# Optimization experiments

Hardware: AMD Instinct MI355X
Metric: run time of the kernel (lower is better)

## Reference

```python
import jax, jax.numpy as jnp
import numpy as np

N_NODES = 50_000
N_EDGES = 1_600_000
N_VMS = 10_000
N_SCORE = 1_000_000
D_IN, D_E, D_OUT = 128, 64, 64
MLP_IN, MLP_H, MLP_OUT = 64, 128, 64
H1, H2 = 50, 25  # GNNTower fixed hidden widths


def setup_inputs() -> dict:
    key = jax.random.key(0)
    ks = jax.random.split(key, 24)
    w = lambda k, s: (jax.random.normal(k, s, jnp.float32) * 0.05)
    return {
        "component_features": jax.random.normal(ks[0], (N_NODES, D_IN), jnp.float32),
        "component_edges_features": jax.random.normal(ks[1], (N_EDGES, D_E), jnp.float32),
        "vm_features": jax.random.normal(ks[2], (N_VMS, MLP_IN), jnp.float32),
        "src": jax.random.randint(ks[3], (N_EDGES,), 0, N_NODES, jnp.int32),
        "dst": jax.random.randint(ks[4], (N_EDGES,), 0, N_NODES, jnp.int32),
        "e_comp": jax.random.randint(ks[5], (N_SCORE,), 0, N_NODES, jnp.int32),
        "e_vm": jax.random.randint(ks[6], (N_SCORE,), 0, N_VMS, jnp.int32),
        # GNN layer 1: W_msg [D_IN+D_E, H1], W_apply [D_IN+H1, H1]
        "Wm1": w(ks[7], (D_IN + D_E, H1)), "bm1": jnp.zeros((H1,), jnp.float32),
        "Wa1": w(ks[8], (D_IN + H1, H1)), "ba1": jnp.zeros((H1,), jnp.float32),
        # GNN layer 2
        "Wm2": w(ks[9], (H1 + D_E, H2)), "bm2": jnp.zeros((H2,), jnp.float32),
        "Wa2": w(ks[10], (H1 + H2, H2)), "ba2": jnp.zeros((H2,), jnp.float32),
        # GNN layer 3
        "Wm3": w(ks[11], (H2 + D_E, D_OUT)), "bm3": jnp.zeros((D_OUT,), jnp.float32),
        "Wa3": w(ks[12], (H2 + D_OUT, D_OUT)), "ba3": jnp.zeros((D_OUT,), jnp.float32),
        # MLP tower
        "Wmlp1": w(ks[13], (MLP_IN, MLP_H)), "bmlp1": jnp.zeros((MLP_H,), jnp.float32),
        "Wmlp2": w(ks[14], (MLP_H, MLP_OUT)), "bmlp2": jnp.zeros((MLP_OUT,), jnp.float32),
    }


def reference(component_features, component_edges_features, vm_features,
              src, dst, e_comp, e_vm,
              Wm1, bm1, Wa1, ba1, Wm2, bm2, Wa2, ba2, Wm3, bm3, Wa3, ba3,
              Wmlp1, bmlp1, Wmlp2, bmlp2):
    ef = component_edges_features

    def gnn_layer(h, Wm, bm, Wa, ba):
        d = h.shape[-1]
        # message: relu(W_msg @ concat(h[src], efeat)) == gather + split matmul (avoids concat copy)
        m = jax.nn.relu(h[src] @ Wm[:d] + ef @ Wm[d:] + bm)  # [E, out]
        # scatter-sum aggregation into destination nodes
        h_neigh = jax.ops.segment_sum(m, dst, num_segments=N_NODES)  # [N, out]
        # apply: relu(W_apply @ concat(h, h_neigh))
        return jax.nn.relu(h @ Wa[:d] + h_neigh @ Wa[d:] + ba)

    h = gnn_layer(component_features, Wm1, bm1, Wa1, ba1)   # [N, 50]
    h = gnn_layer(h, Wm2, bm2, Wa2, ba2)                    # [N, 25]  (dropout = identity in eval)
    h = gnn_layer(h, Wm3, bm3, Wa3, ba3)                    # [N, D_OUT]

    vm = jax.nn.relu(vm_features @ Wmlp1 + bmlp1) @ Wmlp2 + bmlp2  # [V, MLP_OUT]

    # sum over concat(comp_emb[e_comp], vm_emb[e_vm]) == sum of parts
    scores = jnp.sum(h, axis=-1)[e_comp] + jnp.sum(vm, axis=-1)[e_vm]  # [N_SCORE]
    return jax.nn.sigmoid(scores)
```

## Files before the change

### kernel.cpp

```cpp
#include <hip/hip_runtime.h>

typedef unsigned int uint;
typedef unsigned short ushort;
typedef short bf16x8 __attribute__((ext_vector_type(8)));
typedef float f32x4  __attribute__((ext_vector_type(4)));


__device__ __forceinline__ ushort f2bf(float f) {
    uint u = __float_as_uint(f);
    u += 0x7FFFu + ((u >> 16) & 1u);
    return (ushort)(u >> 16);
}
__device__ __forceinline__ uint cvtpk(float lo, float hi) {
    uint r;
    asm("v_cvt_pk_bf16_f32 %0, %1, %2" : "=v"(r) : "v"(lo), "v"(hi));
    return r;
}

template<int K0, int KP0, int K1, int KP1, int KC, int OUT, int WOUT,
         int NTC, int RPT, int MODE>
__global__ __launch_bounds__(256) void tile_gemm(
    const float* __restrict__ X0, int sx0,
    const float* __restrict__ X1, int sx1,
    const float* __restrict__ Wg, const float* __restrict__ Bg,
    float* __restrict__ Y, int sy, int nR)
{
    constexpr int KPT  = KP0 + KP1;
    constexpr int C4   = KC / 4;
    constexpr int OUTP = 4 * NTC;
    constexpr int NTR  = 256 / NTC;
    constexpr int TR   = NTR * RPT;
    static_assert(TR == 128, "tile must be 128 rows");
    static_assert(KPT % KC == 0, "KC must divide KPT");

    __shared__ float4 Xl[TR * C4];
    __shared__ float4 Wl[KC * NTC];
    __shared__ float  __align__(16) bl[OUTP];

    const int tid = threadIdx.x;
    const int r0  = blockIdx.x * TR;

    for (int idx = tid; idx < OUTP; idx += 256)
        bl[idx] = (Bg != nullptr && idx < OUT) ? Bg[idx] : 0.f;

    const int tc  = tid & (NTC - 1);
    const int tr  = tid / NTC;
    const int key = (RPT * tr) >> 3;

    float4 acc[RPT];
    #pragma unroll
    for (int i = 0; i < RPT; i++) acc[i] = make_float4(0.f, 0.f, 0.f, 0.f);

    for (int kc0 = 0; kc0 < KPT; kc0 += KC) {
        if (kc0 != 0) __syncthreads();
        for (int idx = tid; idx < TR * C4; idx += 256) {
            int r = idx / C4, c = idx - r * C4;
            int col = kc0 + 4 * c;
            int gr = r0 + r;
            float4 v = make_float4(0.f, 0.f, 0.f, 0.f);
            if (gr < nR) {
                if (KP1 == 0 || col < KP0)
                    v = *reinterpret_cast<const float4*>(X0 + (long long)gr * sx0 + col);
                else
                    v = *reinterpret_cast<const float4*>(X1 + (long long)gr * sx1 + (col - KP0));
            }
            int cs = c + ((r >> 3) % C4); if (cs >= C4) cs -= C4;
            Xl[r * C4 + cs] = v;
        }
        for (int idx = tid; idx < KC * OUTP; idx += 256) {
            int kl = idx / OUTP, o = idx - kl * OUTP;
            int k = kc0 + kl;
            float v = 0.f;
            if (o < OUT) {
                if (k < KP0) { if (k < K0) v = Wg[k * OUT + o]; }
                else { int kk = k - KP0; if (kk < K1) v = Wg[(K0 + kk) * OUT + o]; }
            }
            ((float*)Wl)[kl * OUTP + o] = v;
        }
        __syncthreads();

        const int km = key % C4;
        #pragma unroll 4
        for (int k4 = 0; k4 < C4; k4++) {
            int cs = k4 + km; if (cs >= C4) cs -= C4;
            float4 x[RPT];
            #pragma unroll
            for (int i = 0; i < RPT; i++)
                x[i] = Xl[(RPT * tr + i) * C4 + cs];
            #pragma unroll
            for (int kk = 0; kk < 4; kk++) {
                float4 w = Wl[(4 * k4 + kk) * NTC + tc];
                #pragma unroll
                for (int i = 0; i < RPT; i++) {
                    float xs = (kk == 0) ? x[i].x : (kk == 1) ? x[i].y
                             : (kk == 2) ? x[i].z : x[i].w;
                    acc[i].x = fmaf(xs, w.x, acc[i].x);
                    acc[i].y = fmaf(xs, w.y, acc[i].y);
                    acc[i].z = fmaf(xs, w.z, acc[i].z);
                    acc[i].w = fmaf(xs, w.w, acc[i].w);
                }
            }
        }
    }

    const float4 b4 = reinterpret_cast<float4*>(bl)[tc];
    const int o = 4 * tc;

    if (MODE == 0 || MODE == 1) {
        if (o < WOUT) {
            #pragma unroll
            for (int i = 0; i < RPT; i++) {
                int gr = r0 + RPT * tr + i;
                if (gr < nR) {
                    float4 v;
                    v.x = acc[i].x + b4.x; v.y = acc[i].y + b4.y;
                    v.z = acc[i].z + b4.z; v.w = acc[i].w + b4.w;
                    if (MODE == 1) {
                        v.x = fmaxf(v.x, 0.f); v.y = fmaxf(v.y, 0.f);
                        v.z = fmaxf(v.z, 0.f); v.w = fmaxf(v.w, 0.f);
                    }
                    *reinterpret_cast<float4*>(Y + (long long)gr * sy + o) = v;
                }
            }
        }
    } else {
        #pragma unroll
        for (int i = 0; i < RPT; i++) {
            int gr = r0 + RPT * tr + i;
            float s = fmaxf(acc[i].x + b4.x, 0.f) + fmaxf(acc[i].y + b4.y, 0.f)
                    + fmaxf(acc[i].z + b4.z, 0.f) + fmaxf(acc[i].w + b4.w, 0.f);
            #pragma unroll
            for (int off = 1; off < NTC; off <<= 1) s += __shfl_xor(s, off);
            if (tc == 0 && gr < nR) Y[gr] = s;
        }
    }
}

__device__ __forceinline__ void proj_stage_A(
    ushort* Al, const float* __restrict__ ef, const int* __restrict__ perm,
    int r0, int nE, int tid)
{
    int row = tid >> 2;
    int kq  = (tid & 3) << 4;
    int gr  = r0 + row;
    long long e = (gr < nE) ? (long long)perm[gr] : 0;
    const float* p = ef + e * 64 + kq;
    float4 f0 = *reinterpret_cast<const float4*>(p);
    float4 f1 = *reinterpret_cast<const float4*>(p + 4);
    float4 f2 = *reinterpret_cast<const float4*>(p + 8);
    float4 f3 = *reinterpret_cast<const float4*>(p + 12);
    ushort u[16];
    u[0]=f2bf(f0.x); u[1]=f2bf(f0.y); u[2]=f2bf(f0.z); u[3]=f2bf(f0.w);
    u[4]=f2bf(f1.x); u[5]=f2bf(f1.y); u[6]=f2bf(f1.z); u[7]=f2bf(f1.w);
    u[8]=f2bf(f2.x); u[9]=f2bf(f2.y); u[10]=f2bf(f2.z); u[11]=f2bf(f2.w);
    u[12]=f2bf(f3.x); u[13]=f2bf(f3.y); u[14]=f2bf(f3.z); u[15]=f2bf(f3.w);
    int kc0 = ((kq >> 3) + 0) ^ (row & 7);
    int kc1 = ((kq >> 3) + 1) ^ (row & 7);
    *reinterpret_cast<bf16x8*>(&Al[(row << 6) + kc0 * 8]) = *reinterpret_cast<bf16x8*>(u);
    *reinterpret_cast<bf16x8*>(&Al[(row << 6) + kc1 * 8]) = *reinterpret_cast<bf16x8*>(u + 8);
}

__global__ __launch_bounds__(256) void proj_fused(
    const float* __restrict__ ef,
    const float* __restrict__ W1e, const float* __restrict__ W2e,
    const float* __restrict__ W3e, const int* __restrict__ perm,
    ushort* __restrict__ G1, ushort* __restrict__ G2, ushort* __restrict__ G3,
    int nE)
{
    constexpr int NT = 10;
    __shared__ ushort Al[64 * 64];
    __shared__ ushort Bl[NT * 128 * 8];

    const int tid = threadIdx.x;

    for (int idx = tid; idx < NT * 128; idx += 256) {
        int t  = idx >> 7;
        int ks = (idx >> 6) & 1;
        int l  = idx & 63;
        int gp  = t * 16 + (l & 15);
        int kb  = ks * 32 + ((l >> 4) << 3);
        ushort u[8];
        #pragma unroll
        for (int j = 0; j < 8; j++) {
            int k = kb + j;
            float w = 0.f;
            if (gp < 64)      { if (gp < 50) w = W1e[k * 50 + gp]; }
            else if (gp < 96) { int c = gp - 64; if (c < 25) w = W2e[k * 25 + c]; }
            else              { int c = gp - 96; w = W3e[k * 64 + c]; }
            u[j] = f2bf(w);
        }
        *reinterpret_cast<bf16x8*>(&Bl[idx * 8]) = *reinterpret_cast<bf16x8*>(u);
    }

    const int wv = tid >> 6;
    const int l  = tid & 63;
    const int ntiles = (nE + 63) >> 6;

    for (int tile = blockIdx.x; tile < ntiles; tile += gridDim.x) {
        const int r0 = tile << 6;
        __syncthreads();
        proj_stage_A(Al, ef, perm, r0, nE, tid);
        __syncthreads();

        f32x4 acc[NT];
        #pragma unroll
        for (int t = 0; t < NT; t++) acc[t] = (f32x4){0.f, 0.f, 0.f, 0.f};
        const int rl = wv * 16 + (l & 15);
        #pragma unroll
        for (int ks = 0; ks < 2; ks++) {
            int kch = (ks * 4 + (l >> 4)) ^ (rl & 7);
            bf16x8 a = *reinterpret_cast<const bf16x8*>(&Al[(rl << 6) + kch * 8]);
            #pragma unroll
            for (int t = 0; t < NT; t++) {
                bf16x8 b = *reinterpret_cast<const bf16x8*>(&Bl[((t * 2 + ks) * 64 + l) * 8]);
                acc[t] = __builtin_amdgcn_mfma_f32_16x16x32_bf16(a, b, acc[t], 0, 0, 0);
            }
        }

        const int grpS = (r0 >> 2) + (wv << 2) + (l >> 4);
        const int pos0 = grpS << 2;
        const bool v01 = (pos0 < nE);
        const bool v23 = (pos0 + 2 < nE);
        const int c = l & 15;
        #pragma unroll
        for (int t = 0; t < NT; t++) {
            uint p01 = cvtpk(acc[t][0], acc[t][1]);
            uint p23 = cvtpk(acc[t][2], acc[t][3]);
            ushort* Gp; size_t idx;
            if (t < 4)      { Gp = G1; idx = (size_t)grpS * 256 + (t * 16 + c) * 4; }
            else if (t < 6) { Gp = G2; idx = (size_t)grpS * 128 + ((t - 4) * 16 + c) * 4; }
            else            { Gp = G3; idx = (size_t)grpS * 256 + ((t - 6) * 16 + c) * 4; }
            if (v01) *reinterpret_cast<uint*>(Gp + idx)     = p01;
            if (v23) *reinterpret_cast<uint*>(Gp + idx + 2) = p23;
        }
    }
}

template<int NT, int GS>
__global__ __launch_bounds__(256) void proj_single(
    const float* __restrict__ ef,
    const float* __restrict__ W, int wcols,
    const int* __restrict__ perm, ushort* __restrict__ G, int nE)
{
    __shared__ ushort Al[64 * 64];
    __shared__ ushort Bl[NT * 128 * 8];

    const int tid = threadIdx.x;

    for (int idx = tid; idx < NT * 128; idx += 256) {
        int t  = idx >> 7;
        int ks = (idx >> 6) & 1;
        int l  = idx & 63;
        int col = t * 16 + (l & 15);
        int kb  = ks * 32 + ((l >> 4) << 3);
        ushort u[8];
        #pragma unroll
        for (int j = 0; j < 8; j++) {
            int k = kb + j;
            float w = (col < wcols) ? W[k * wcols + col] : 0.f;
            u[j] = f2bf(w);
        }
        *reinterpret_cast<bf16x8*>(&Bl[idx * 8]) = *reinterpret_cast<bf16x8*>(u);
    }

    const int wv = tid >> 6;
    const int l  = tid & 63;
    const int ntiles = (nE + 63) >> 6;

    for (int tile = blockIdx.x; tile < ntiles; tile += gridDim.x) {
        const int r0 = tile << 6;
        __syncthreads();
        proj_stage_A(Al, ef, perm, r0, nE, tid);
        __syncthreads();

        f32x4 acc[NT];
        #pragma unroll
        for (int t = 0; t < NT; t++) acc[t] = (f32x4){0.f, 0.f, 0.f, 0.f};
        const int rl = wv * 16 + (l & 15);
        #pragma unroll
        for (int ks = 0; ks < 2; ks++) {
            int kch = (ks * 4 + (l >> 4)) ^ (rl & 7);
            bf16x8 a = *reinterpret_cast<const bf16x8*>(&Al[(rl << 6) + kch * 8]);
            #pragma unroll
            for (int t = 0; t < NT; t++) {
                bf16x8 b = *reinterpret_cast<const bf16x8*>(&Bl[((t * 2 + ks) * 64 + l) * 8]);
                acc[t] = __builtin_amdgcn_mfma_f32_16x16x32_bf16(a, b, acc[t], 0, 0, 0);
            }
        }

        const int grpS = (r0 >> 2) + (wv << 2) + (l >> 4);
        const int pos0 = grpS << 2;
        const bool v01 = (pos0 < nE);
        const bool v23 = (pos0 + 2 < nE);
        const int c = l & 15;
        #pragma unroll
        for (int t = 0; t < NT; t++) {
            uint p01 = cvtpk(acc[t][0], acc[t][1]);
            uint p23 = cvtpk(acc[t][2], acc[t][3]);
            size_t idx = (size_t)grpS * (GS * 4) + (t * 16 + c) * 4;
            if (v01) *reinterpret_cast<uint*>(G + idx)     = p01;
            if (v23) *reinterpret_cast<uint*>(G + idx + 2) = p23;
        }
    }
}

template<int NCL, int GS, int SP>
__global__ __launch_bounds__(256) void agg_csr(
    const ushort* __restrict__ G, const int* __restrict__ srcp,
    const int* __restrict__ rowp, const float* __restrict__ P,
    float* __restrict__ ng, int nN)
{
    const int o = threadIdx.x & (NCL - 1);
    const int g = threadIdx.x / NCL;
    const int n = blockIdx.x * (256 / NCL) + g;
    if (n >= nN) return;
    const int s0 = rowp[n], s1 = rowp[n + 1];

    float a[8];
    #pragma unroll
    for (int j = 0; j < 8; j++) a[j] = 0.f;

    if (s0 < s1) {
        const int g0 = s0 >> 2, g1 = (s1 - 1) >> 2;
        for (int grp = g0; grp <= g1; grp++) {
            const ushort* gb = G + (size_t)grp * (GS * 4) + o * 32;
            uint4 c0 = *reinterpret_cast<const uint4*>(gb);
            uint4 c1 = *reinterpret_cast<const uint4*>(gb + 8);
            uint4 c2 = *reinterpret_cast<const uint4*>(gb + 16);
            uint4 c3 = *reinterpret_cast<const uint4*>(gb + 24);
            int4 s4 = *reinterpret_cast<const int4*>(srcp + grp * 4);
            const int rlo = s0 - grp * 4;
            const int rhi = s1 - grp * 4;
            #pragma unroll
            for (int r = 0; r < 4; r++) {
                if (r < rlo || r >= rhi) continue;
                const int s = (r == 0) ? s4.x : (r == 1) ? s4.y : (r == 2) ? s4.z : s4.w;
                const float* pp = P + (size_t)s * SP + o * 8;
                float4 pa = *reinterpret_cast<const float4*>(pp);
                float4 pb = *reinterpret_cast<const float4*>(pp + 4);
                #pragma unroll
                for (int k = 0; k < 8; k++) {
                    uint lo, hi;
                    switch (k) {
                        case 0: lo = c0.x; hi = c0.y; break;
                        case 1: lo = c0.z; hi = c0.w; break;
                        case 2: lo = c1.x; hi = c1.y; break;
                        case 3: lo = c1.z; hi = c1.w; break;
                        case 4: lo = c2.x; hi = c2.y; break;
                        case 5: lo = c2.z; hi = c2.w; break;
                        case 6: lo = c3.x; hi = c3.y; break;
                        default: lo = c3.z; hi = c3.w; break;
                    }
                    const uint q = (r & 2) ? hi : lo;
                    const uint v = (r & 1) ? (q & 0xffff0000u) : (q << 16);
                    const float pv = (k == 0) ? pa.x : (k == 1) ? pa.y
                                   : (k == 2) ? pa.z : (k == 3) ? pa.w
                                   : (k == 4) ? pb.x : (k == 5) ? pb.y
                                   : (k == 6) ? pb.z : pb.w;
                    a[k] += fmaxf(pv + __uint_as_float(v), 0.f);
                }
            }
        }
    }
    float4 w0 = {a[0], a[1], a[2], a[3]}, w1 = {a[4], a[5], a[6], a[7]};
    float* yp = ng + (size_t)n * 64 + o * 8;
    *reinterpret_cast<float4*>(yp)     = w0;
    *reinterpret_cast<float4*>(yp + 4) = w1;
}

__global__ __launch_bounds__(256) void hist_kernel(
    const int* __restrict__ dst, int* __restrict__ deg, int nE)
{
    for (int e = blockIdx.x * 256 + threadIdx.x; e < nE; e += gridDim.x * 256)
        atomicAdd(&deg[dst[e]], 1);
}

__global__ __launch_bounds__(256) void scan_blksum(
    const int* __restrict__ deg, int* __restrict__ bsum, int nN)
{
    const int t = threadIdx.x;
    const int base = blockIdx.x * 1024;
    int s = 0;
    for (int i = t; i < 1024; i += 256) {
        int id = base + i;
        s += (id < nN) ? deg[id] : 0;
    }
    #pragma unroll
    for (int off = 32; off > 0; off >>= 1) s += __shfl_down(s, off);
    __shared__ int w[4];
    if ((t & 63) == 0) w[t >> 6] = s;
    __syncthreads();
    if (t == 0) bsum[blockIdx.x] = w[0] + w[1] + w[2] + w[3];
}

__global__ __launch_bounds__(256) void scan_top(
    int* __restrict__ bsum, int nB, int* __restrict__ rowp, int nN)
{
    const int t = threadIdx.x;
    int v = (t < nB) ? bsum[t] : 0;
    int x = v;
    #pragma unroll
    for (int off = 1; off < 64; off <<= 1) {
        int u = __shfl_up(x, off);
        if ((t & 63) >= off) x += u;
    }
    __shared__ int wsum[4];
    if ((t & 63) == 63) wsum[t >> 6] = x;
    __syncthreads();
    int add = 0;
    #pragma unroll
    for (int i = 0; i < 4; i++) if (i < (t >> 6)) add += wsum[i];
    x += add;
    if (t < nB) bsum[t] = x - v;
    if (t == nB - 1) rowp[nN] = x;
}

__global__ __launch_bounds__(256) void scan_final(
    const int* __restrict__ deg, const int* __restrict__ bsum,
    int* __restrict__ rowp, int nN)
{
    const int t = threadIdx.x;
    const int idx0 = blockIdx.x * 1024 + t * 4;
    int e[4];
    #pragma unroll
    for (int i = 0; i < 4; i++) {
        int id = idx0 + i;
        e[i] = (id < nN) ? deg[id] : 0;
    }
    int tl = e[0] + e[1] + e[2] + e[3];
    int x = tl;
    #pragma unroll
    for (int off = 1; off < 64; off <<= 1) {
        int u = __shfl_up(x, off);
        if ((t & 63) >= off) x += u;
    }
    __shared__ int wsum[4];
    if ((t & 63) == 63) wsum[t >> 6] = x;
    __syncthreads();
    int add = 0;
    #pragma unroll
    for (int i = 0; i < 4; i++) if (i < (t >> 6)) add += wsum[i];
    int run = (x - tl) + add + bsum[blockIdx.x];
    #pragma unroll
    for (int i = 0; i < 4; i++) {
        int id = idx0 + i;
        if (id < nN) rowp[id] = run;
        run += e[i];
    }
}

__global__ __launch_bounds__(256) void scatter_kernel(
    const int* __restrict__ src, const int* __restrict__ dst,
    const int* __restrict__ rowp, int* __restrict__ cursor,
    int* __restrict__ srcp, int* __restrict__ perm, int nE)
{
    for (int e = blockIdx.x * 256 + threadIdx.x; e < nE; e += gridDim.x * 256) {
        int d = dst[e];
        int pos = rowp[d] + atomicAdd(&cursor[d], 1);
        srcp[pos] = src[e];
        perm[pos] = e;
    }
}

__global__ __launch_bounds__(256) void vm_kernel(
    const float* __restrict__ vmf, const float* __restrict__ W1,
    const float* __restrict__ b1, const float* __restrict__ W2,
    const float* __restrict__ b2, float* __restrict__ vm_sum, int nV)
{
    __shared__ float w2s[132];
    const int tid = threadIdx.x;
    if (tid < 128) {
        float s = 0.f;
        for (int o = 0; o < 64; o++) s += W2[tid * 64 + o];
        w2s[tid] = s;
    } else if (tid == 128) {
        float bs = 0.f;
        for (int o = 0; o < 64; o++) bs += b2[o];
        w2s[128] = bs;
    }
    __syncthreads();

    const int lane = tid & 63;
    const int grp  = tid >> 6;
    for (int v = blockIdx.x * 4 + grp; v < nV; v += gridDim.x * 4) {
        const float* vr = vmf + (long long)v * 64;
        float a0 = b1[lane], a1 = b1[lane + 64];
        #pragma unroll 4
        for (int k = 0; k < 64; k += 4) {
            float4 x = *reinterpret_cast<const float4*>(vr + k);
            a0 = fmaf(x.x, W1[(k + 0) * 128 + lane], a0);
            a0 = fmaf(x.y, W1[(k + 1) * 128 + lane], a0);
            a0 = fmaf(x.z, W1[(k + 2) * 128 + lane], a0);
            a0 = fmaf(x.w, W1[(k + 3) * 128 + lane], a0);
            a1 = fmaf(x.x, W1[(k + 0) * 128 + lane + 64], a1);
            a1 = fmaf(x.y, W1[(k + 1) * 128 + lane + 64], a1);
            a1 = fmaf(x.z, W1[(k + 2) * 128 + lane + 64], a1);
            a1 = fmaf(x.w, W1[(k + 3) * 128 + lane + 64], a1);
        }
        float part = fmaxf(a0, 0.f) * w2s[lane] + fmaxf(a1, 0.f) * w2s[lane + 64];
        #pragma unroll
        for (int off = 32; off > 0; off >>= 1) part += __shfl_down(part, off);
        if (lane == 0) vm_sum[v] = part + w2s[128];
    }
}

__global__ __launch_bounds__(256) void score_kernel(
    const int* __restrict__ ec, const int* __restrict__ ev,
    const float* __restrict__ ns, const float* __restrict__ vs,
    float* __restrict__ out, int n)
{
    int i = blockIdx.x * blockDim.x + threadIdx.x;
    if (i < n) {
        float x = ns[ec[i]] + vs[ev[i]];
        out[i] = 1.f / (1.f + expf(-x));
    }
}

extern "C" void kernel_launch(void* const* d_in, const int* in_sizes, int n_in,
                              void* d_out, int out_size, void* d_ws, size_t ws_size,
                              hipStream_t stream)
{
    const float* comp = (const float*)d_in[0];
    const float* ef   = (const float*)d_in[1];
    const float* vmf  = (const float*)d_in[2];
    const int*   src  = (const int*)d_in[3];
    const int*   dst  = (const int*)d_in[4];
    const int*   ecmp = (const int*)d_in[5];
    const int*   evm  = (const int*)d_in[6];
    const float* Wm1 = (const float*)d_in[7];  const float* bm1 = (const float*)d_in[8];
    const float* Wa1 = (const float*)d_in[9];  const float* ba1 = (const float*)d_in[10];
    const float* Wm2 = (const float*)d_in[11]; const float* bm2 = (const float*)d_in[12];
    const float* Wa2 = (const float*)d_in[13]; const float* ba2 = (const float*)d_in[14];
    const float* Wm3 = (const float*)d_in[15]; const float* bm3 = (const float*)d_in[16];
    const float* Wa3 = (const float*)d_in[17]; const float* ba3 = (const float*)d_in[18];
    const float* W1  = (const float*)d_in[19]; const float* b1  = (const float*)d_in[20];
    const float* W2  = (const float*)d_in[21]; const float* b2  = (const float*)d_in[22];

    const int nN = in_sizes[0] / 128;
    const int nE = in_sizes[3];
    const int nV = in_sizes[2] / 64;
    const int nS = in_sizes[5];
    const int nE4 = (nE + 63) & ~63;

    float* ws = (float*)d_ws;
    float* bufA     = ws;
    float* bufB     = bufA + (size_t)nN * 64;
    float* ng       = bufB + (size_t)nN * 64;
    float* node_sum = ng + (size_t)nN * 64;
    float* vm_sum   = node_sum + nN;
    int*   iws      = (int*)(((size_t)(vm_sum + nV) + 15) & ~(size_t)15);
    int*   deg      = iws;
    int*   cursor   = deg + nN;
    int*   rowp     = cursor + nN;
    int*   bsum     = rowp + nN + 1;
    int*   srcp     = (int*)(((size_t)(bsum + 256) + 15) & ~(size_t)15);
    int*   perm     = srcp + nE;
    size_t Goff = (((size_t)((char*)(perm + nE) - (char*)d_ws)) + 255) & ~(size_t)255;
    ushort* G1 = (ushort*)((char*)d_ws + Goff);
    const size_t g1u = (size_t)nE4 * 64, g2u = (size_t)nE4 * 32, g3u = (size_t)nE4 * 64;
    const bool single = (Goff + (g1u + g2u + g3u) * 2) <= ws_size;
    ushort* G2 = single ? (G1 + g1u) : G1;
    ushort* G3 = single ? (G2 + g2u) : G1;

    float* h1 = bufA;
    float* h2 = bufB;
    float* P1 = bufB;
    float* P2 = bufB;
    float* P3 = bufA;

    const float* We1 = Wm1 + 128 * 50;
    const float* We2 = Wm2 + 50 * 25;
    const float* We3 = Wm3 + 25 * 64;

    const int ngrid  = (nN + 127) / 128;
    const int ptiles = nE4 / 64;
    const int pgrid  = ptiles < 2048 ? ptiles : 2048;
    const int a8grid = (nN * 8 + 255) / 256;
    const int a4grid = (nN * 4 + 255) / 256;
    const int sgrid  = (nE + 255) / 256 < 4096 ? (nE + 255) / 256 : 4096;
    const int nB     = (nN + 1023) / 1024;
    const int vgrid  = ((nV + 3) / 4) < 640 ? ((nV + 3) / 4) : 640;

    hipMemsetAsync(deg, 0, (size_t)(2 * nN) * sizeof(int), stream);
    hist_kernel<<<sgrid, 256, 0, stream>>>(dst, deg, nE);
    scan_blksum<<<nB, 256, 0, stream>>>(deg, bsum, nN);
    scan_top<<<1, 256, 0, stream>>>(bsum, nB, rowp, nN);
    scan_final<<<nB, 256, 0, stream>>>(deg, bsum, rowp, nN);
    scatter_kernel<<<sgrid, 256, 0, stream>>>(src, dst, rowp, cursor, srcp, perm, nE);

    if (single)
        proj_fused<<<pgrid, 256, 0, stream>>>(ef, We1, We2, We3, perm, G1, G2, G3, nE);
    else
        proj_single<4, 64><<<pgrid, 256, 0, stream>>>(ef, We1, 50, perm, G1, nE);

    tile_gemm<128,128, 0,0, 64, 50, 64, 16, 8, 0><<<ngrid, 256, 0, stream>>>(
        comp, 128, nullptr, 0, Wm1, bm1, P1, 64, nN);
    agg_csr<8, 64, 64><<<a8grid, 256, 0, stream>>>(G1, srcp, rowp, P1, ng, nN);
    if (!single)
        proj_single<2, 32><<<pgrid, 256, 0, stream>>>(ef, We2, 25, perm, G2, nE);
    tile_gemm<128,128, 50,52, 60, 50, 52, 16, 8, 1><<<ngrid, 256, 0, stream>>>(
        comp, 128, ng, 64, Wa1, ba1, h1, 52, nN);

    tile_gemm<50,52, 0,0, 52, 25, 32, 8, 4, 0><<<ngrid, 256, 0, stream>>>(
        h1, 52, nullptr, 0, Wm2, bm2, P2, 32, nN);
    agg_csr<4, 32, 32><<<a4grid, 256, 0, stream>>>(G2, srcp, rowp, P2, ng, nN);
    if (!single)
        proj_single<4, 64><<<pgrid, 256, 0, stream>>>(ef, We3, 64, perm, G3, nE);
    tile_gemm<50,52, 25,28, 80, 25, 28, 8, 4, 1><<<ngrid, 256, 0, stream>>>(
        h1, 52, ng, 64, Wa2, ba2, h2, 28, nN);

    tile_gemm<25,28, 0,0, 28, 64, 64, 16, 8, 0><<<ngrid, 256, 0, stream>>>(
        h2, 28, nullptr, 0, Wm3, bm3, P3, 64, nN);
    agg_csr<8, 64, 64><<<a8grid, 256, 0, stream>>>(G3, srcp, rowp, P3, ng, nN);
    tile_gemm<25,28, 64,68, 48, 64, 64, 16, 8, 2><<<ngrid, 256, 0, stream>>>(
        h2, 28, ng, 64, Wa3, ba3, node_sum, 1, nN);

    vm_kernel<<<vgrid, 256, 0, stream>>>(vmf, W1, b1, W2, b2, vm_sum, nV);
    score_kernel<<<(nS + 255) / 256, 256, 0, stream>>>(ecmp, evm, node_sum, vm_sum, (float*)d_out, nS);
}
```

Before: 808.4 us.

## Fuse apply GEMM with next layer's message pre-projection; prefetch edge tiles

Adds a fused kernel that computes a GNN layer's apply output, keeps the tile in shared memory, and immediately multiplies it by the next layer's message weights. This removes two separate node-level GEMM launches and the re-read of h1/h2 from global memory. The edge projection kernels now prefetch the next tile's edge features into registers while the MFMA work runs, which raises register pressure. Their bounds-guarded packed stores are replaced with a single unguarded uint2 store per fragment. That store can run past nE on the last partial tile unless the G buffers are padded.

Result: faster. 789.7 us (-2.3%).

```diff
diff --git a/kernel.cpp b/kernel.cpp
--- a/kernel.cpp
+++ b/kernel.cpp
@@ -136,8 +136,163 @@
     }
 }
 
-__device__ __forceinline__ void proj_stage_A(
-    ushort* Al, const float* __restrict__ ef, const int* __restrict__ perm,
+template<int K0, int KP0, int K1, int KP1, int KC, int OUT1, int WOUT1,
+         int OUT1P, int SY1, int OUT2, int OUT2P, int SY2,
+         int NTC, int RPT, int NTC2, int RPT2>
+__global__ __launch_bounds__(256) void fused_apply_pre(
+    const float* __restrict__ X0, int sx0,
+    const float* __restrict__ X1, int sx1,
+    const float* __restrict__ Wa, const float* __restrict__ ba,
+    const float* __restrict__ Wm, const float* __restrict__ bm,
+    float* __restrict__ Y1, float* __restrict__ Y2, int nR)
+{
+    constexpr int KPT  = KP0 + KP1;
+    constexpr int C4   = KC / 4;
+    constexpr int OUTP = 4 * NTC;
+    constexpr int NTR  = 256 / NTC;
+    constexpr int TR   = NTR * RPT;
+    constexpr int BLSZ = (OUTP > OUT2P) ? OUTP : OUT2P;
+    static_assert(TR == 128, "tile must be 128 rows");
+    static_assert(KPT % KC == 0, "KC must divide KPT");
+    static_assert((256 / NTC2) * RPT2 == 128, "phase2 covers 128 rows");
+    static_assert(OUT2P == 4 * NTC2, "phase2 col tiling");
+    static_assert(128 * OUT1P <= TR * C4 * 4, "Hl fits in Xl");
+    static_assert(OUT1 * OUT2P <= KC * NTC * 4, "Wm fits in Wl");
+
+    __shared__ float4 Xl[TR * C4];
+    __shared__ float4 Wl[KC * NTC];
+    __shared__ float  __align__(16) bl[BLSZ];
+    float* Hl = (float*)Xl;
+
+    const int tid = threadIdx.x;
+    const int r0  = blockIdx.x * TR;
+
+    for (int idx = tid; idx < OUTP; idx += 256)
+        bl[idx] = (idx < OUT1) ? ba[idx] : 0.f;
+
+    const int tc  = tid & (NTC - 1);
+    const int tr  = tid / NTC;
+    const int key = (RPT * tr) >> 3;
+
+    float4 acc[RPT];
+    #pragma unroll
+    for (int i = 0; i < RPT; i++) acc[i] = make_float4(0.f, 0.f, 0.f, 0.f);
+
+    for (int kc0 = 0; kc0 < KPT; kc0 += KC) {
+        if (kc0 != 0) __syncthreads();
+        for (int idx = tid; idx < TR * C4; idx += 256) {
+            int r = idx / C4, c = idx - r * C4;
+            int col = kc0 + 4 * c;
+            int gr = r0 + r;
+            float4 v = make_float4(0.f, 0.f, 0.f, 0.f);
+            if (gr < nR) {
+                if (KP1 == 0 || col < KP0)
+                    v = *reinterpret_cast<const float4*>(X0 + (long long)gr * sx0 + col);
+                else
+                    v = *reinterpret_cast<const float4*>(X1 + (long long)gr * sx1 + (col - KP0));
+            }
+            int cs = c + ((r >> 3) % C4); if (cs >= C4) cs -= C4;
+            Xl[r * C4 + cs] = v;
+        }
+        for (int idx = tid; idx < KC * OUTP; idx += 256) {
+            int kl = idx / OUTP, o = idx - kl * OUTP;
+            int k = kc0 + kl;
+            float v = 0.f;
+            if (o < OUT1) {
+                if (k < KP0) { if (k < K0) v = Wa[k * OUT1 + o]; }
+                else { int kk = k - KP0; if (kk < K1) v = Wa[(K0 + kk) * OUT1 + o]; }
+            }
+            ((float*)Wl)[kl * OUTP + o] = v;
+        }
+        __syncthreads();
+
+        const int km = key % C4;
+        #pragma unroll 4
+        for (int k4 = 0; k4 < C4; k4++) {
+            int cs = k4 + km; if (cs >= C4) cs -= C4;
+            float4 x[RPT];
+            #pragma unroll
+            for (int i = 0; i < RPT; i++)
+                x[i] = Xl[(RPT * tr + i) * C4 + cs];
+            #pragma unroll
+            for (int kk = 0; kk < 4; kk++) {
+                float4 w = Wl[(4 * k4 + kk) * NTC + tc];
+                #pragma unroll
+                for (int i = 0; i < RPT; i++) {
+                    float xs = (kk == 0) ? x[i].x : (kk == 1) ? x[i].y
+                             : (kk == 2) ? x[i].z : x[i].w;
+                    acc[i].x = fmaf(xs, w.x, acc[i].x);
+                    acc[i].y = fmaf(xs, w.y, acc[i].y);
+                    acc[i].z = fmaf(xs, w.z, acc[i].z);
+                    acc[i].w = fmaf(xs, w.w, acc[i].w);
+                }
+            }
+        }
+    }
+
+    const float4 b4 = reinterpret_cast<float4*>(bl)[tc];
+    const int o = 4 * tc;
+
+    __syncthreads();
+
+    if (o < WOUT1) {
+        #pragma unroll
+        for (int i = 0; i < RPT; i++) {
+            int lr = RPT * tr + i;
+            int gr = r0 + lr;
+            float4 v;
+            v.x = fmaxf(acc[i].x + b4.x, 0.f); v.y = fmaxf(acc[i].y + b4.y, 0.f);
+            v.z = fmaxf(acc[i].z + b4.z, 0.f); v.w = fmaxf(acc[i].w + b4.w, 0.f);
+            if (gr >= nR) v = make_float4(0.f, 0.f, 0.f, 0.f);
+            if (o < OUT1P)
+                *reinterpret_cast<float4*>(Hl + lr * OUT1P + o) = v;
+            if (gr < nR)
+                *reinterpret_cast<float4*>(Y1 + (long long)gr * SY1 + o) = v;
+        }
+    }
+    for (int idx = tid; idx < OUT1 * OUT2P; idx += 256) {
+        int k = idx / OUT2P, oc = idx - k * OUT2P;
+        ((float*)Wl)[idx] = (oc < OUT2) ? Wm[k * OUT2 + oc] : 0.f;
+    }
+    for (int idx = tid; idx < OUT2P; idx += 256)
+        bl[idx] = (idx < OUT2) ? bm[idx] : 0.f;
+    __syncthreads();
+
+    const int tc2 = tid & (NTC2 - 1);
+    const int tr2 = tid / NTC2;
+    float4 acc2[RPT2];
+    #pragma unroll
+    for (int i = 0; i < RPT2; i++) acc2[i] = make_float4(0.f, 0.f, 0.f, 0.f);
+
+    #pragma unroll 4
+    for (int k = 0; k < OUT1; k++) {
+        float4 w = reinterpret_cast<float4*>((float*)Wl)[k * NTC2 + tc2];
+        #pragma unroll
+        for (int i = 0; i < RPT2; i++) {
+            float xs = Hl[(RPT2 * tr2 + i) * OUT1P + k];
+            acc2[i].x = fmaf(xs, w.x, acc2[i].x);
+            acc2[i].y = fmaf(xs, w.y, acc2[i].y);
+            acc2[i].z = fmaf(xs, w.z, acc2[i].z);
+            acc2[i].w = fmaf(xs, w.w, acc2[i].w);
+        }
+    }
+    const float4 b2 = reinterpret_cast<float4*>(bl)[tc2];
+    #pragma unroll
+    for (int i = 0; i < RPT2; i++) {
+        int gr = r0 + RPT2 * tr2 + i;
+        if (gr < nR) {
+            float4 v;
+            v.x = acc2[i].x + b2.x; v.y = acc2[i].y + b2.y;
+            v.z = acc2[i].z + b2.z; v.w = acc2[i].w + b2.w;
+            *reinterpret_cast<float4*>(Y2 + (long long)gr * SY2 + 4 * tc2) = v;
+        }
+    }
+}
+
+struct AFrag { float4 f0, f1, f2, f3; };
+
+__device__ __forceinline__ AFrag proj_load_A(
+    const float* __restrict__ ef, const int* __restrict__ perm,
     int r0, int nE, int tid)
 {
     int row = tid >> 2;
@@ -145,15 +300,23 @@
     int gr  = r0 + row;
     long long e = (gr < nE) ? (long long)perm[gr] : 0;
     const float* p = ef + e * 64 + kq;
-    float4 f0 = *reinterpret_cast<const float4*>(p);
-    float4 f1 = *reinterpret_cast<const float4*>(p + 4);
-    float4 f2 = *reinterpret_cast<const float4*>(p + 8);
-    float4 f3 = *reinterpret_cast<const float4*>(p + 12);
+    AFrag a;
+    a.f0 = *reinterpret_cast<const float4*>(p);
+    a.f1 = *reinterpret_cast<const float4*>(p + 4);
+    a.f2 = *reinterpret_cast<const float4*>(p + 8);
+    a.f3 = *reinterpret_cast<const float4*>(p + 12);
+    return a;
+}
+
+__device__ __forceinline__ void proj_write_A(ushort* Al, const AFrag& a, int tid)
+{
+    int row = tid >> 2;
+    int kq  = (tid & 3) << 4;
     ushort u[16];
-    u[0]=f2bf(f0.x); u[1]=f2bf(f0.y); u[2]=f2bf(f0.z); u[3]=f2bf(f0.w);
-    u[4]=f2bf(f1.x); u[5]=f2bf(f1.y); u[6]=f2bf(f1.z); u[7]=f2bf(f1.w);
-    u[8]=f2bf(f2.x); u[9]=f2bf(f2.y); u[10]=f2bf(f2.z); u[11]=f2bf(f2.w);
-    u[12]=f2bf(f3.x); u[13]=f2bf(f3.y); u[14]=f2bf(f3.z); u[15]=f2bf(f3.w);
+    u[0]=f2bf(a.f0.x); u[1]=f2bf(a.f0.y); u[2]=f2bf(a.f0.z); u[3]=f2bf(a.f0.w);
+    u[4]=f2bf(a.f1.x); u[5]=f2bf(a.f1.y); u[6]=f2bf(a.f1.z); u[7]=f2bf(a.f1.w);
+    u[8]=f2bf(a.f2.x); u[9]=f2bf(a.f2.y); u[10]=f2bf(a.f2.z); u[11]=f2bf(a.f2.w);
+    u[12]=f2bf(a.f3.x); u[13]=f2bf(a.f3.y); u[14]=f2bf(a.f3.z); u[15]=f2bf(a.f3.w);
     int kc0 = ((kq >> 3) + 0) ^ (row & 7);
     int kc1 = ((kq >> 3) + 1) ^ (row & 7);
     *reinterpret_cast<bf16x8*>(&Al[(row << 6) + kc0 * 8]) = *reinterpret_cast<bf16x8*>(u);
@@ -196,11 +359,17 @@
     const int l  = tid & 63;
     const int ntiles = (nE + 63) >> 6;
 
-    for (int tile = blockIdx.x; tile < ntiles; tile += gridDim.x) {
+    int tile = blockIdx.x;
+    AFrag a;
+    if (tile < ntiles) a = proj_load_A(ef, perm, tile << 6, nE, tid);
+
+    for (; tile < ntiles; tile += gridDim.x) {
         const int r0 = tile << 6;
         __syncthreads();
-        proj_stage_A(Al, ef, perm, r0, nE, tid);
+        proj_write_A(Al, a, tid);
         __syncthreads();
+        int nxt = tile + gridDim.x;
+        if (nxt < ntiles) a = proj_load_A(ef, perm, nxt << 6, nE, tid);
 
         f32x4 acc[NT];
         #pragma unroll
@@ -209,29 +378,26 @@
         #pragma unroll
         for (int ks = 0; ks < 2; ks++) {
             int kch = (ks * 4 + (l >> 4)) ^ (rl & 7);
-            bf16x8 a = *reinterpret_cast<const bf16x8*>(&Al[(rl << 6) + kch * 8]);
+            bf16x8 av = *reinterpret_cast<const bf16x8*>(&Al[(rl << 6) + kch * 8]);
             #pragma unroll
             for (int t = 0; t < NT; t++) {
                 bf16x8 b = *reinterpret_cast<const bf16x8*>(&Bl[((t * 2 + ks) * 64 + l) * 8]);
-                acc[t] = __builtin_amdgcn_mfma_f32_16x16x32_bf16(a, b, acc[t], 0, 0, 0);
+                acc[t] = __builtin_amdgcn_mfma_f32_16x16x32_bf16(av, b, acc[t], 0, 0, 0);
             }
         }
 
         const int grpS = (r0 >> 2) + (wv << 2) + (l >> 4);
-        const int pos0 = grpS << 2;
-        const bool v01 = (pos0 < nE);
-        const bool v23 = (pos0 + 2 < nE);
         const int c = l & 15;
         #pragma unroll
         for (int t = 0; t < NT; t++) {
-            uint p01 = cvtpk(acc[t][0], acc[t][1]);
-            uint p23 = cvtpk(acc[t][2], acc[t][3]);
+            uint2 pq;
+            pq.x = cvtpk(acc[t][0], acc[t][1]);
+            pq.y = cvtpk(acc[t][2], acc[t][3]);
             ushort* Gp; size_t idx;
             if (t < 4)      { Gp = G1; idx = (size_t)grpS * 256 + (t * 16 + c) * 4; }
             else if (t < 6) { Gp = G2; idx = (size_t)grpS * 128 + ((t - 4) * 16 + c) * 4; }
             else            { Gp = G3; idx = (size_t)grpS * 256 + ((t - 6) * 16 + c) * 4; }
-            if (v01) *reinterpret_cast<uint*>(Gp + idx)     = p01;
-            if (v23) *reinterpret_cast<uint*>(Gp + idx + 2) = p23;
+            *reinterpret_cast<uint2*>(Gp + idx) = pq;
         }
     }
 }
@@ -267,11 +433,17 @@
     const int l  = tid & 63;
     const int ntiles = (nE + 63) >> 6;
 
-    for (int tile = blockIdx.x; tile < ntiles; tile += gridDim.x) {
+    int tile = blockIdx.x;
+    AFrag a;
+    if (tile < ntiles) a = proj_load_A(ef, perm, tile << 6, nE, tid);
+
+    for (; tile < ntiles; tile += gridDim.x) {
         const int r0 = tile << 6;
         __syncthreads();
-        proj_stage_A(Al, ef, perm, r0, nE, tid);
+        proj_write_A(Al, a, tid);
         __syncthreads();
+        int nxt = tile + gridDim.x;
+        if (nxt < ntiles) a = proj_load_A(ef, perm, nxt << 6, nE, tid);
 
         f32x4 acc[NT];
         #pragma unroll
@@ -280,26 +452,23 @@
         #pragma unroll
         for (int ks = 0; ks < 2; ks++) {
             int kch = (ks * 4 + (l >> 4)) ^ (rl & 7);
-            bf16x8 a = *reinterpret_cast<const bf16x8*>(&Al[(rl << 6) + kch * 8]);
+            bf16x8 av = *reinterpret_cast<const bf16x8*>(&Al[(rl << 6) + kch * 8]);
             #pragma unroll
             for (int t = 0; t < NT; t++) {
                 bf16x8 b = *reinterpret_cast<const bf16x8*>(&Bl[((t * 2 + ks) * 64 + l) * 8]);
-                acc[t] = __builtin_amdgcn_mfma_f32_16x16x32_bf16(a, b, acc[t], 0, 0, 0);
+                acc[t] = __builtin_amdgcn_mfma_f32_16x16x32_bf16(av, b, acc[t], 0, 0, 0);
             }
         }
 
         const int grpS = (r0 >> 2) + (wv << 2) + (l >> 4);
-        const int pos0 = grpS << 2;
-        const bool v01 = (pos0 < nE);
-        const bool v23 = (pos0 + 2 < nE);
         const int c = l & 15;
         #pragma unroll
         for (int t = 0; t < NT; t++) {
-            uint p01 = cvtpk(acc[t][0], acc[t][1]);
-            uint p23 = cvtpk(acc[t][2], acc[t][3]);
+            uint2 pq;
+            pq.x = cvtpk(acc[t][0], acc[t][1]);
+            pq.y = cvtpk(acc[t][2], acc[t][3]);
             size_t idx = (size_t)grpS * (GS * 4) + (t * 16 + c) * 4;
-            if (v01) *reinterpret_cast<uint*>(G + idx)     = p01;
-            if (v23) *reinterpret_cast<uint*>(G + idx + 2) = p23;
+            *reinterpret_cast<uint2*>(G + idx) = pq;
         }
     }
 }
@@ -598,19 +767,15 @@
     agg_csr<8, 64, 64><<<a8grid, 256, 0, stream>>>(G1, srcp, rowp, P1, ng, nN);
     if (!single)
         proj_single<2, 32><<<pgrid, 256, 0, stream>>>(ef, We2, 25, perm, G2, nE);
-    tile_gemm<128,128, 50,52, 60, 50, 52, 16, 8, 1><<<ngrid, 256, 0, stream>>>(
-        comp, 128, ng, 64, Wa1, ba1, h1, 52, nN);
-
-    tile_gemm<50,52, 0,0, 52, 25, 32, 8, 4, 0><<<ngrid, 256, 0, stream>>>(
-        h1, 52, nullptr, 0, Wm2, bm2, P2, 32, nN);
+    fused_apply_pre<128,128, 50,52, 60, 50, 52, 52, 52, 25, 32, 32, 16, 8, 8, 4>
+        <<<ngrid, 256, 0, stream>>>(comp, 128, ng, 64, Wa1, ba1, Wm2, bm2, h1, P2, nN);
+
     agg_csr<4, 32, 32><<<a4grid, 256, 0, stream>>>(G2, srcp, rowp, P2, ng, nN);
     if (!single)
         proj_single<4, 64><<<pgrid, 256, 0, stream>>>(ef, We3, 64, perm, G3, nE);
-    tile_gemm<50,52, 25,28, 80, 25, 28, 8, 4, 1><<<ngrid, 256, 0, stream>>>(
-        h1, 52, ng, 64, Wa2, ba2, h2, 28, nN);
-
-    tile_gemm<25,28, 0,0, 28, 64, 64, 16, 8, 0><<<ngrid, 256, 0, stream>>>(
-        h2, 28, nullptr, 0, Wm3, bm3, P3, 64, nN);
+    fused_apply_pre<50,52, 25,28, 80, 25, 28, 28, 28, 64, 64, 64, 8, 4, 16, 8>
+        <<<ngrid, 256, 0, stream>>>(h1, 52, ng, 64, Wa2, ba2, Wm3, bm3, h2, P3, nN);
+
     agg_csr<8, 64, 64><<<a8grid, 256, 0, stream>>>(G3, srcp, rowp, P3, ng, nN);
     tile_gemm<25,28, 64,68, 48, 64, 64, 16, 8, 2><<<ngrid, 256, 0, stream>>>(
         h2, 28, ng, 64, Wa3, ba3, node_sum, 1, nN);
```
